# Performance work log

Measured on AMD Instinct MI355X. Metric: run time of the kernel, lower is better.

Reference implementation:

```python
import jax, jax.numpy as jnp
import numpy as np


def sign_fn(x):
    # torch.sign(torch.sign(x) + 0.5): maps x >= 0 -> +1, x < 0 -> -1 (zero -> +1)
    return jnp.where(x >= 0, 1.0, -1.0).astype(x.dtype)


def setup_inputs() -> dict:
    key = jax.random.key(0)
    kx, kw, kb = jax.random.split(key, 3)
    TOKENS, IN, OUT = 8192, 4096, 4096
    x = jax.random.normal(kx, (TOKENS, IN), dtype=jnp.float32)
    weight = jax.random.normal(kw, (OUT, IN), dtype=jnp.float32)
    bias = jax.random.normal(kb, (OUT,), dtype=jnp.float32)
    return {"x": x, "weight": weight, "bias": bias}


def reference(x, weight, bias):
    b_weight = sign_fn(weight)  # [out, in], values in {+1, -1}
    b_bias = sign_fn(bias)      # [out]
    # nn.functional.linear: y = x @ W^T + b
    return jnp.einsum('ti,oi->to', x, b_weight) + b_bias
```

## Files before the change

### kernel.cpp

```cpp
#include <hip/hip_runtime.h>


typedef __attribute__((ext_vector_type(4))) int   i32x4;
typedef __attribute__((ext_vector_type(8))) short short8;
typedef __attribute__((ext_vector_type(4))) float f32x4;

constexpr int M = 8192;
constexpr int N = 4096;
constexpr int K = 4096;

constexpr int BM = 256, BN = 256, BK = 64;
constexpr int NTILES = K / BK;
constexpr int TILE_A = BM * BK;
constexpr int TILE_B = BN * BK;
constexpr int BUFSZ  = TILE_A + TILE_B;
constexpr int RING   = 4;

__device__ __forceinline__ void load_lds16(const void* g, void* l) {
    __builtin_amdgcn_global_load_lds(
        (const __attribute__((address_space(1))) unsigned int*)g,
        (__attribute__((address_space(3))) unsigned int*)l, 16, 0, 0);
}

constexpr int WB  = 1024;
constexpr int WCH = N * K / 8;

__global__ __launch_bounds__(256) void prep_fused(
    const float* __restrict__ X, const float* __restrict__ W,
    signed char* __restrict__ Xq, signed char* __restrict__ Wq,
    float* __restrict__ Scale) {
    __shared__ float wmax[4];
    const int t = threadIdx.x;

    if (blockIdx.x < M) {
        const int row = blockIdx.x;
        const float4* xr = reinterpret_cast<const float4*>(X + (size_t)row * K);
        float4 v[4];
        float mx = 0.f;
#pragma unroll
        for (int i = 0; i < 4; ++i) {
            v[i] = xr[t + i * 256];
            mx = fmaxf(mx, fmaxf(fmaxf(fabsf(v[i].x), fabsf(v[i].y)),
                                 fmaxf(fabsf(v[i].z), fabsf(v[i].w))));
        }
#pragma unroll
        for (int off = 32; off > 0; off >>= 1)
            mx = fmaxf(mx, __shfl_down(mx, off));
        if ((t & 63) == 0) wmax[t >> 6] = mx;
        __syncthreads();
        float rmax = fmaxf(fmaxf(wmax[0], wmax[1]), fmaxf(wmax[2], wmax[3]));
        rmax = fmaxf(rmax, 1e-20f);
        const float inv = 127.f / rmax;
        if (t == 0) Scale[row] = rmax * (1.f / 127.f);

        unsigned int* out = reinterpret_cast<unsigned int*>(Xq + (size_t)row * K);
#pragma unroll
        for (int i = 0; i < 4; ++i) {
            int q0 = (int)rintf(v[i].x * inv);
            int q1 = (int)rintf(v[i].y * inv);
            int q2 = (int)rintf(v[i].z * inv);
            int q3 = (int)rintf(v[i].w * inv);
            unsigned int p = (q0 & 255) | ((q1 & 255) << 8) |
                             ((q2 & 255) << 16) | ((unsigned)(q3 & 255) << 24);
            out[t + i * 256] = p;
        }
    } else {
        const float4* W4 = reinterpret_cast<const float4*>(W);
        uint2* O = reinterpret_cast<uint2*>(Wq);
        auto sg = [](float f) -> unsigned int { return (f >= 0.f) ? 1u : 0xFFu; };
        size_t idx = (size_t)(blockIdx.x - M) * 256 + t;
        const size_t stride = (size_t)WB * 256;
        for (size_t c = idx; c < (size_t)WCH; c += stride) {
            float4 a = W4[c * 2], b = W4[c * 2 + 1];
            uint2 o;
            o.x = sg(a.x) | (sg(a.y) << 8) | (sg(a.z) << 16) | (sg(a.w) << 24);
            o.y = sg(b.x) | (sg(b.y) << 8) | (sg(b.z) << 16) | (sg(b.w) << 24);
            O[c] = o;
        }
    }
}

struct GemmCtx {
    const signed char* Abase;
    const signed char* Bbase;
    int voff;
    signed char* lbase;
    int aoff;
    int boff;
};

struct Frags { i32x4 b[4]; i32x4 a[8]; };

__device__ __forceinline__ void stage_full(const GemmCtx& c, int t) {
    signed char* d = c.lbase + (t & (RING - 1)) * BUFSZ;
    const size_t ko = (size_t)t * BK;
    load_lds16(c.Abase + ko + c.voff, d);
    load_lds16(c.Abase + (size_t)128 * K + ko + c.voff, d + 8192);
    load_lds16(c.Bbase + ko + c.voff, d + TILE_A);
    load_lds16(c.Bbase + (size_t)128 * K + ko + c.voff, d + TILE_A + 8192);
}

__device__ __forceinline__ void read_frags(const GemmCtx& c,
                                           const signed char* smem, int t,
                                           Frags& f) {
    const signed char* base = smem + (t & (RING - 1)) * BUFSZ;
#pragma unroll
    for (int ni = 0; ni < 4; ++ni)
        f.b[ni] = *reinterpret_cast<const i32x4*>(base + c.boff + ni * 1024);
#pragma unroll
    for (int mi = 0; mi < 8; ++mi)
        f.a[mi] = *reinterpret_cast<const i32x4*>(base + c.aoff + mi * 1024);
}

__device__ __forceinline__ void do_mfma(const Frags& f, i32x4 (&acc)[8][4]) {
    __builtin_amdgcn_s_setprio(1);
#pragma unroll
    for (int mi = 0; mi < 8; ++mi)
#pragma unroll
        for (int ni = 0; ni < 4; ++ni)
            acc[mi][ni] = __builtin_amdgcn_mfma_i32_16x16x64_i8(
                f.a[mi], f.b[ni], acc[mi][ni], 0, 0, 0);
    __builtin_amdgcn_s_setprio(0);
}

template <int VM, bool STAGE, bool RDNEXT, bool BAR>
__device__ __forceinline__ void kstep(
    const GemmCtx& c, const signed char* smem, int j,
    Frags& cur, Frags& nxt, i32x4 (&acc)[8][4]) {
    if constexpr (STAGE) stage_full(c, j + 3);
    if constexpr (VM >= 0)
        asm volatile("s_waitcnt vmcnt(%0)" :: "i"(VM) : "memory");
    if constexpr (BAR) {
        asm volatile("s_waitcnt lgkmcnt(0)" ::: "memory");
        __builtin_amdgcn_s_barrier();
        asm volatile("" ::: "memory");
    }
    if constexpr (RDNEXT) read_frags(c, smem, j + 1, nxt);
    __builtin_amdgcn_sched_barrier(0);
    do_mfma(cur, acc);
}

__global__ __launch_bounds__(512, 2) void gemm_i8_p(
    const signed char* __restrict__ Aq, const signed char* __restrict__ Bq,
    const float* __restrict__ Scale, const float* __restrict__ Bias,
    float* __restrict__ OUT) {
    __shared__ signed char smem[RING * BUFSZ];

    const int tid  = threadIdx.x;
    const int lane = tid & 63;
    const int w    = tid >> 6;
    const int wm   = w >> 2;
    const int wn   = w & 3;
    const int rl   = lane & 15;
    const int cq16 = (((lane >> 4) ^ ((rl >> 1) & 3)) << 4);

    const int wg  = blockIdx.x;
    const int lin = (wg & 7) * 64 + (wg >> 3);
    const int n0  = (lin & 15) * BN;
    const int m0  = (lin >> 4) * BM;

    const int srow = tid >> 2;
    const int cg   = ((tid & 3) ^ ((srow >> 1) & 3)) * 16;

    GemmCtx c;
    c.Abase = Aq + (size_t)m0 * K;
    c.Bbase = Bq + (size_t)n0 * K;
    c.voff  = srow * K + cg;
    c.lbase = smem + w * 1024;
    c.aoff  = (wm * 128 + rl) * BK + cq16;
    c.boff  = TILE_A + (wn * 64 + rl) * BK + cq16;

    i32x4 acc[8][4];
#pragma unroll
    for (int mi = 0; mi < 8; ++mi)
#pragma unroll
        for (int ni = 0; ni < 4; ++ni)
            acc[mi][ni] = (i32x4){0, 0, 0, 0};

    stage_full(c, 0); stage_full(c, 1); stage_full(c, 2);
    asm volatile("s_waitcnt vmcnt(8)" ::: "memory");
    __builtin_amdgcn_s_barrier();
    asm volatile("" ::: "memory");
    Frags fA, fB;
    read_frags(c, smem, 0, fA);

    for (int j = 0; j < NTILES - 4; j += 2) {
        kstep<8, true, true, true>(c, smem, j,     fA, fB, acc);
        kstep<8, true, true, true>(c, smem, j + 1, fB, fA, acc);
    }
    kstep<8, true,  true,  true >(c, smem, NTILES - 4, fA, fB, acc);
    kstep<4, false, true,  true >(c, smem, NTILES - 3, fB, fA, acc);
    kstep<0, false, true,  true >(c, smem, NTILES - 2, fA, fB, acc);
    kstep<-1, false, false, false>(c, smem, NTILES - 1, fB, fA, acc);

#pragma unroll
    for (int ni = 0; ni < 4; ++ni) {
        const int gcol = n0 + wn * 64 + ni * 16 + rl;
        const float sb = (Bias[gcol] >= 0.f) ? 1.f : -1.f;
#pragma unroll
        for (int mi = 0; mi < 8; ++mi) {
            const int growb = m0 + wm * 128 + mi * 16 + (lane >> 4) * 4;
            const float4 sc = *reinterpret_cast<const float4*>(&Scale[growb]);
            OUT[(size_t)(growb + 0) * N + gcol] = (float)acc[mi][ni][0] * sc.x + sb;
            OUT[(size_t)(growb + 1) * N + gcol] = (float)acc[mi][ni][1] * sc.y + sb;
            OUT[(size_t)(growb + 2) * N + gcol] = (float)acc[mi][ni][2] * sc.z + sb;
            OUT[(size_t)(growb + 3) * N + gcol] = (float)acc[mi][ni][3] * sc.w + sb;
        }
    }
}

constexpr int MT   = 128;
constexpr int NTF  = 128;
constexpr int LDSS = 40;
constexpr int KTB  = 32;
__device__ __forceinline__ unsigned short f2b(float f) {
    unsigned int u = __builtin_bit_cast(unsigned int, f);
    u += 0x7FFFu + ((u >> 16) & 1u);
    return (unsigned short)(u >> 16);
}
__global__ __launch_bounds__(256) void binlin_fallback(
    const float* __restrict__ X, const float* __restrict__ W,
    const float* __restrict__ B, float* __restrict__ OUT) {
    __shared__ unsigned short As[MT][LDSS];
    __shared__ unsigned short Bs[NTF][LDSS];
    const int tid  = threadIdx.x;
    const int lane = tid & 63;
    const int wave = tid >> 6;
    const int wm   = wave >> 1;
    const int wn   = wave & 1;
    const int m0 = blockIdx.y * MT;
    const int n0 = blockIdx.x * NTF;
    const int rl = lane & 15;
    const int kq = (lane >> 4) * 8;
    f32x4 acc[4][4];
#pragma unroll
    for (int mi = 0; mi < 4; ++mi)
#pragma unroll
        for (int ni = 0; ni < 4; ++ni)
            acc[mi][ni] = (f32x4){0.f, 0.f, 0.f, 0.f};
    for (int k0 = 0; k0 < K; k0 += KTB) {
#pragma unroll
        for (int it = 0; it < 4; ++it) {
            int g = tid + it * 256, row = g >> 3, c4 = (g & 7) << 2;
            float4 v = *reinterpret_cast<const float4*>(&X[(size_t)(m0 + row) * K + k0 + c4]);
            ushort4 h;
            h.x = f2b(v.x); h.y = f2b(v.y); h.z = f2b(v.z); h.w = f2b(v.w);
            *reinterpret_cast<ushort4*>(&As[row][c4]) = h;
        }
#pragma unroll
        for (int it = 0; it < 4; ++it) {
            int g = tid + it * 256, row = g >> 3, c4 = (g & 7) << 2;
            float4 v = *reinterpret_cast<const float4*>(&W[(size_t)(n0 + row) * K + k0 + c4]);
            ushort4 h;
            h.x = (v.x >= 0.f) ? 0x3F80u : 0xBF80u;
            h.y = (v.y >= 0.f) ? 0x3F80u : 0xBF80u;
            h.z = (v.z >= 0.f) ? 0x3F80u : 0xBF80u;
            h.w = (v.w >= 0.f) ? 0x3F80u : 0xBF80u;
            *reinterpret_cast<ushort4*>(&Bs[row][c4]) = h;
        }
        __syncthreads();
        short8 a[4], b[4];
#pragma unroll
        for (int mi = 0; mi < 4; ++mi)
            a[mi] = *reinterpret_cast<const short8*>(&As[wm * 64 + mi * 16 + rl][kq]);
#pragma unroll
        for (int ni = 0; ni < 4; ++ni)
            b[ni] = *reinterpret_cast<const short8*>(&Bs[wn * 64 + ni * 16 + rl][kq]);
#pragma unroll
        for (int mi = 0; mi < 4; ++mi)
#pragma unroll
            for (int ni = 0; ni < 4; ++ni)
                acc[mi][ni] = __builtin_amdgcn_mfma_f32_16x16x32_bf16(
                    a[mi], b[ni], acc[mi][ni], 0, 0, 0);
        __syncthreads();
    }
#pragma unroll
    for (int ni = 0; ni < 4; ++ni) {
        int gcol = n0 + wn * 64 + ni * 16 + rl;
        float sb = (B[gcol] >= 0.f) ? 1.f : -1.f;
#pragma unroll
        for (int mi = 0; mi < 4; ++mi) {
            int growb = m0 + wm * 64 + mi * 16 + (lane >> 4) * 4;
#pragma unroll
            for (int r = 0; r < 4; ++r)
                OUT[(size_t)(growb + r) * N + gcol] = acc[mi][ni][r] + sb;
        }
    }
}

extern "C" void kernel_launch(void* const* d_in, const int* in_sizes, int n_in,
                              void* d_out, int out_size, void* d_ws, size_t ws_size,
                              hipStream_t stream) {
    const float* x  = (const float*)d_in[0];
    const float* w  = (const float*)d_in[1];
    const float* b  = (const float*)d_in[2];
    float* out      = (float*)d_out;

    const size_t need = (size_t)M * K + (size_t)N * K + (size_t)M * sizeof(float);
    if (ws_size >= need) {
        signed char* Xq = (signed char*)d_ws;
        signed char* Wq = Xq + (size_t)M * K;
        float* Scale    = (float*)(Wq + (size_t)N * K);

        prep_fused<<<dim3(M + WB), dim3(256), 0, stream>>>(x, w, Xq, Wq, Scale);
        gemm_i8_p<<<dim3((M / BM) * (N / BN)), dim3(512), 0, stream>>>(
            Xq, Wq, Scale, b, out);
    } else {
        dim3 grid(N / NTF, M / MT);
        binlin_fallback<<<grid, dim3(256), 0, stream>>>(x, w, b, out);
    }
}
```

Baseline: 416.3 us.

## Reorder k-step pipeline to read fragments before MFMA and deepen prefetch

Each k-step now issues the next tile's LDS fragment reads first, then the MFMA block, then the global-to-LDS stage for tile j+4. It waits on vmcnt/lgkmcnt and the barrier only at the end of the step, and the ring prefetch depth grows from three tiles to four. The LDS reads are written in inline asm with immediate offsets from precomputed 32-bit LDS addresses. The aim is to overlap LDS read latency and global loads with MFMA work and to cut address arithmetic. The cost is that staging tile j+4 writes into the same ring slot as tile j, which is only safe because the MFMAs consume register copies. Inline asm also hides the LDS reads from the compiler's dependency tracking, so correctness rests on the manual waitcnts.

```diff
diff --git a/kernel.cpp b/kernel.cpp
--- a/kernel.cpp
+++ b/kernel.cpp
@@ -85,8 +85,8 @@
     const signed char* Bbase;
     int voff;
     signed char* lbase;
-    int aoff;
-    int boff;
+    unsigned baseA;
+    unsigned baseB;
 };
 
 struct Frags { i32x4 b[4]; i32x4 a[8]; };
@@ -100,16 +100,25 @@
     load_lds16(c.Bbase + (size_t)128 * K + ko + c.voff, d + TILE_A + 8192);
 }
 
-__device__ __forceinline__ void read_frags(const GemmCtx& c,
-                                           const signed char* smem, int t,
-                                           Frags& f) {
-    const signed char* base = smem + (t & (RING - 1)) * BUFSZ;
-#pragma unroll
-    for (int ni = 0; ni < 4; ++ni)
-        f.b[ni] = *reinterpret_cast<const i32x4*>(base + c.boff + ni * 1024);
-#pragma unroll
-    for (int mi = 0; mi < 8; ++mi)
-        f.a[mi] = *reinterpret_cast<const i32x4*>(base + c.aoff + mi * 1024);
+__device__ __forceinline__ void read_frags_asm(unsigned aA, unsigned aB,
+                                               Frags& f) {
+    asm volatile(
+        "ds_read_b128 %0, %12 offset:0\n\t"
+        "ds_read_b128 %1, %12 offset:1024\n\t"
+        "ds_read_b128 %2, %12 offset:2048\n\t"
+        "ds_read_b128 %3, %12 offset:3072\n\t"
+        "ds_read_b128 %4, %13 offset:0\n\t"
+        "ds_read_b128 %5, %13 offset:1024\n\t"
+        "ds_read_b128 %6, %13 offset:2048\n\t"
+        "ds_read_b128 %7, %13 offset:3072\n\t"
+        "ds_read_b128 %8, %13 offset:4096\n\t"
+        "ds_read_b128 %9, %13 offset:5120\n\t"
+        "ds_read_b128 %10, %13 offset:6144\n\t"
+        "ds_read_b128 %11, %13 offset:7168"
+        : "=&v"(f.b[0]), "=&v"(f.b[1]), "=&v"(f.b[2]), "=&v"(f.b[3]),
+          "=&v"(f.a[0]), "=&v"(f.a[1]), "=&v"(f.a[2]), "=&v"(f.a[3]),
+          "=&v"(f.a[4]), "=&v"(f.a[5]), "=&v"(f.a[6]), "=&v"(f.a[7])
+        : "v"(aB), "v"(aA));
 }
 
 __device__ __forceinline__ void do_mfma(const Frags& f, i32x4 (&acc)[8][4]) {
@@ -125,19 +134,19 @@
 
 template <int VM, bool STAGE, bool RDNEXT, bool BAR>
 __device__ __forceinline__ void kstep(
-    const GemmCtx& c, const signed char* smem, int j,
-    Frags& cur, Frags& nxt, i32x4 (&acc)[8][4]) {
-    if constexpr (STAGE) stage_full(c, j + 3);
+    const GemmCtx& c, int j, Frags& cur, Frags& nxt, i32x4 (&acc)[8][4]) {
+    if constexpr (RDNEXT) {
+        const unsigned ring = (unsigned)(((j + 1) & (RING - 1)) * BUFSZ);
+        read_frags_asm(c.baseA + ring, c.baseB + ring, nxt);
+    }
+    __builtin_amdgcn_sched_barrier(0);
+    do_mfma(cur, acc);
+    if constexpr (STAGE) stage_full(c, j + 4);
     if constexpr (VM >= 0)
         asm volatile("s_waitcnt vmcnt(%0)" :: "i"(VM) : "memory");
-    if constexpr (BAR) {
-        asm volatile("s_waitcnt lgkmcnt(0)" ::: "memory");
-        __builtin_amdgcn_s_barrier();
-        asm volatile("" ::: "memory");
-    }
-    if constexpr (RDNEXT) read_frags(c, smem, j + 1, nxt);
+    asm volatile("s_waitcnt lgkmcnt(0)" ::: "memory");
     __builtin_amdgcn_sched_barrier(0);
-    do_mfma(cur, acc);
+    if constexpr (BAR) __builtin_amdgcn_s_barrier();
 }
 
 __global__ __launch_bounds__(512, 2) void gemm_i8_p(
@@ -167,8 +176,9 @@
     c.Bbase = Bq + (size_t)n0 * K;
     c.voff  = srow * K + cg;
     c.lbase = smem + w * 1024;
-    c.aoff  = (wm * 128 + rl) * BK + cq16;
-    c.boff  = TILE_A + (wn * 64 + rl) * BK + cq16;
+    const unsigned lds0 = (unsigned)(unsigned long long)&smem[0];
+    c.baseA = lds0 + (unsigned)((wm * 128 + rl) * BK + cq16);
+    c.baseB = lds0 + (unsigned)(TILE_A + (wn * 64 + rl) * BK + cq16);
 
     i32x4 acc[8][4];
 #pragma unroll
@@ -177,21 +187,23 @@
         for (int ni = 0; ni < 4; ++ni)
             acc[mi][ni] = (i32x4){0, 0, 0, 0};
 
-    stage_full(c, 0); stage_full(c, 1); stage_full(c, 2);
+    stage_full(c, 0); stage_full(c, 1); stage_full(c, 2); stage_full(c, 3);
     asm volatile("s_waitcnt vmcnt(8)" ::: "memory");
     __builtin_amdgcn_s_barrier();
-    asm volatile("" ::: "memory");
     Frags fA, fB;
-    read_frags(c, smem, 0, fA);
+    read_frags_asm(c.baseA, c.baseB, fA);
+    asm volatile("s_waitcnt lgkmcnt(0)" ::: "memory");
+    __builtin_amdgcn_sched_barrier(0);
+    __builtin_amdgcn_s_barrier();
 
     for (int j = 0; j < NTILES - 4; j += 2) {
-        kstep<8, true, true, true>(c, smem, j,     fA, fB, acc);
-        kstep<8, true, true, true>(c, smem, j + 1, fB, fA, acc);
-    }
-    kstep<8, true,  true,  true >(c, smem, NTILES - 4, fA, fB, acc);
-    kstep<4, false, true,  true >(c, smem, NTILES - 3, fB, fA, acc);
-    kstep<0, false, true,  true >(c, smem, NTILES - 2, fA, fB, acc);
-    kstep<-1, false, false, false>(c, smem, NTILES - 1, fB, fA, acc);
+        kstep<8, true, true, true>(c, j,     fA, fB, acc);
+        kstep<8, true, true, true>(c, j + 1, fB, fA, acc);
+    }
+    kstep<4,  false, true,  true >(c, NTILES - 4, fA, fB, acc);
+    kstep<0,  false, true,  true >(c, NTILES - 3, fB, fA, acc);
+    kstep<-1, false, true,  false>(c, NTILES - 2, fA, fB, acc);
+    kstep<-1, false, false, false>(c, NTILES - 1, fB, fA, acc);
 
 #pragma unroll
     for (int ni = 0; ni < 4; ++ni) {
```

After: 402.5 us. 1.03x faster.
